# Kernel optimization log

Hardware: AMD Instinct MI355X
Metric: run time of the kernel (lower is better)

Reference implementation:

```python
import jax, jax.numpy as jnp
import numpy as np

NUM_HEADS = 8
NUM_GROUPS = 8
EPS = 1e-5


def group_norm(x, weight, bias):
    B, C, T, H, W = x.shape
    xg = x.reshape(B, NUM_GROUPS, C // NUM_GROUPS, T, H, W)
    mean = xg.mean(axis=(2, 3, 4, 5), keepdims=True)
    var = xg.var(axis=(2, 3, 4, 5), keepdims=True)
    xg = (xg - mean) * jax.lax.rsqrt(var + EPS)
    x = xg.reshape(B, C, T, H, W)
    return x * weight[None, :, None, None, None] + bias[None, :, None, None, None]


def setup_inputs() -> dict:
    key = jax.random.key(0)
    ks = jax.random.split(key, 5)
    B, C, T, H, W = 4, 512, 16, 32, 32
    x = jax.random.normal(ks[0], (B, C, T, H, W), dtype=jnp.float32)
    gn_weight = jnp.ones((C,), dtype=jnp.float32)
    gn_bias = jnp.zeros((C,), dtype=jnp.float32)
    # 1x1x1 Conv3d weights collapse to dense (out, in) matrices
    qkv_w = jax.random.normal(ks[1], (3 * C, C), dtype=jnp.float32) * (1.0 / np.sqrt(C))
    qkv_b = jax.random.normal(ks[2], (3 * C,), dtype=jnp.float32) * 0.02
    out_w = jax.random.normal(ks[3], (C, C), dtype=jnp.float32) * (1.0 / np.sqrt(C))
    out_b = jax.random.normal(ks[4], (C,), dtype=jnp.float32) * 0.02
    return {"x": x, "gn_weight": gn_weight, "gn_bias": gn_bias,
            "qkv_w": qkv_w, "qkv_b": qkv_b, "out_w": out_w, "out_b": out_b}


def reference(x, gn_weight, gn_bias, qkv_w, qkv_b, out_w, out_b):
    B, C, T, H, W = x.shape
    nh = NUM_HEADS
    d = C // nh
    N = T * H * W

    h = group_norm(x, gn_weight, gn_bias)

    # 1x1x1 conv == pointwise channel matmul
    hf = h.reshape(B, C, N)                                  # [B, C, N]
    qkv = jnp.einsum('oc,bcn->bon', qkv_w, hf) + qkv_b[None, :, None]
    q, k, v = jnp.split(qkv, 3, axis=1)                      # each [B, C, N]
    q = q.reshape(B, nh, d, N)
    k = k.reshape(B, nh, d, N)
    v = v.reshape(B, nh, d, N)

    # NOTE: faithful to the torch code — contraction is over N (tokens),
    # giving a [B, nh, d, d] channel-attention matrix; softmax over last d.
    scale = d ** (-0.5)
    attn = jnp.einsum('bhdn,bhen->bhde', q, k) * scale       # [B, nh, d, d]
    attn = jax.nn.softmax(attn, axis=-1)
    out = jnp.einsum('bhde,bhen->bhdn', attn, v)             # [B, nh, d, N]

    out = out.reshape(B, C, N)
    out = jnp.einsum('oc,bcn->bon', out_w, out) + out_b[None, :, None]
    out = out.reshape(B, C, T, H, W)
    return x + out
```

## Files before the change

### kernel.cpp

```cpp
#include <hip/hip_runtime.h>
#include <hip/hip_fp16.h>


#define CCH 512
#define NTOK 16384
#define NHEAD 8

typedef _Float16 f16;
typedef _Float16 f16x8 __attribute__((ext_vector_type(8)));
typedef float f32x4 __attribute__((ext_vector_type(4)));

__device__ __forceinline__ void g2l16(const void* g, void* l) {
  __builtin_amdgcn_global_load_lds((const __attribute__((address_space(1))) void*)g,
                                   (__attribute__((address_space(3))) void*)l,
                                   16, 0, 0);
}

__global__ __launch_bounds__(256) void k_cast2(const float* __restrict__ srcA,
                                               f16* __restrict__ dstA,
                                               const float* __restrict__ srcB,
                                               f16* __restrict__ dstB) {
  int i = blockIdx.x * 256 + threadIdx.x;
  int n4 = blockIdx.y ? (CCH * CCH / 4) : (3 * CCH * CCH / 4);
  const float* src = blockIdx.y ? srcB : srcA;
  f16* dst = blockIdx.y ? dstB : dstA;
  if (i < n4) {
    float4 v = *(const float4*)&src[i * 4];
    f16 h[4] __attribute__((aligned(8)));
    h[0] = (f16)v.x; h[1] = (f16)v.y; h[2] = (f16)v.z; h[3] = (f16)v.w;
    *(uint2*)&dst[i * 4] = *(const uint2*)h;
  }
}

__global__ __launch_bounds__(256) void k_wvt(const float* __restrict__ qkvw,
                                             f16* __restrict__ Wvt16) {
  int et = blockIdx.x, ct = blockIdx.y;
  __shared__ f16 tl[64][72];
  int t = threadIdx.x;
  int r = t >> 2, cq = (t & 3) * 16;
  const float* src = &qkvw[(size_t)(1024 + et * 64 + r) * CCH + ct * 64 + cq];
#pragma unroll
  for (int k = 0; k < 4; ++k) {
    float4 v = *(const float4*)(src + k * 4);
    tl[r][cq + k * 4 + 0] = (f16)v.x; tl[r][cq + k * 4 + 1] = (f16)v.y;
    tl[r][cq + k * 4 + 2] = (f16)v.z; tl[r][cq + k * 4 + 3] = (f16)v.w;
  }
  __syncthreads();
  f16 hv[16] __attribute__((aligned(16)));
#pragma unroll
  for (int j = 0; j < 16; ++j) hv[j] = tl[cq + j][r];
  f16* dst = &Wvt16[(size_t)(ct * 64 + r) * CCH + et * 64 + cq];
  *(uint4*)&dst[0] = ((const uint4*)hv)[0];
  *(uint4*)&dst[8] = ((const uint4*)hv)[1];
}

__global__ __launch_bounds__(256) void k_stats(const float* __restrict__ x,
                                               float* __restrict__ stats) {
  int bg = blockIdx.y;
  int chunk = blockIdx.x;
  const float4* p = (const float4*)(x + (size_t)bg * (64ull * NTOK)) + (size_t)chunk * 8192;
  float s = 0.f, q = 0.f;
  for (int i = threadIdx.x; i < 8192; i += 256) {
    float4 v = p[i];
    s += v.x + v.y + v.z + v.w;
    q += v.x * v.x + v.y * v.y + v.z * v.z + v.w * v.w;
  }
  for (int off = 32; off; off >>= 1) { s += __shfl_down(s, off); q += __shfl_down(q, off); }
  __shared__ float ls[4], lq[4];
  int wid = threadIdx.x >> 6, lane = threadIdx.x & 63;
  if (lane == 0) { ls[wid] = s; lq[wid] = q; }
  __syncthreads();
  if (threadIdx.x == 0) {
    atomicAdd(&stats[bg * 2 + 0], ls[0] + ls[1] + ls[2] + ls[3]);
    atomicAdd(&stats[bg * 2 + 1], lq[0] + lq[1] + lq[2] + lq[3]);
  }
}

__global__ __launch_bounds__(256) void k_gnorm(const float* __restrict__ x,
                                               const float* __restrict__ gw,
                                               const float* __restrict__ gb,
                                               const float* __restrict__ stats,
                                               f16* __restrict__ H, f16* __restrict__ Ht,
                                               float* __restrict__ svec) {
  int nc = blockIdx.x;
  int cg = blockIdx.y;
  int b = blockIdx.z;
  int t = threadIdx.x;
  __shared__ f16 T2[64][260];
  __shared__ float svp[4][64];
  float sum = stats[(b * 8 + cg) * 2], sq = stats[(b * 8 + cg) * 2 + 1];
  const float inv = 1.f / (64.f * (float)NTOK);
  float mean = sum * inv;
  float var = fmaxf(sq * inv - mean * mean, 0.f);
  float rsig = rsqrtf(var + 1e-5f);
  int c0 = cg * 64, n0 = nc * 256;
  int tq = t & 63, rr0 = t >> 6;
#pragma unroll
  for (int it = 0; it < 16; ++it) {
    int r = it * 4 + rr0;
    int c = c0 + r;
    float a = gw[c] * rsig;
    float bb = gb[c] - mean * a;
    size_t idx = ((size_t)(b * CCH + c)) * NTOK + n0 + tq * 4;
    float4 xv = *(const float4*)&x[idx];
    f16 hh[4] __attribute__((aligned(8)));
    hh[0] = (f16)(xv.x * a + bb);
    hh[1] = (f16)(xv.y * a + bb);
    hh[2] = (f16)(xv.z * a + bb);
    hh[3] = (f16)(xv.w * a + bb);
    *(uint2*)&H[idx] = *(const uint2*)hh;
    *(uint2*)&T2[r][tq * 4] = *(const uint2*)hh;
  }
  __syncthreads();
  {
    int c = t & 63, q = t >> 6;
    float acc = 0.f;
#pragma unroll
    for (int j = 0; j < 64; ++j) acc += (float)T2[c][q * 64 + j];
    svp[q][c] = acc;
  }
  __syncthreads();
  if (t < 64) {
    atomicAdd(&svec[b * CCH + c0 + t],
              svp[0][t] + svp[1][t] + svp[2][t] + svp[3][t]);
  }
  int s8 = t & 7, nl = t >> 3;
#pragma unroll
  for (int it = 0; it < 8; ++it) {
    int n = it * 32 + nl;
    f16 g[8] __attribute__((aligned(16)));
#pragma unroll
    for (int j = 0; j < 8; ++j) g[j] = T2[s8 * 8 + j][n];
    *(uint4*)&Ht[((size_t)b * NTOK + n0 + n) * CCH + c0 + s8 * 8] = *(const uint4*)g;
  }
}

#define SPLITS 16
__global__ __launch_bounds__(256, 2) void k_syrk(const f16* __restrict__ H,
                                                 float* __restrict__ G) {
  const int TI[10] = {0, 0, 0, 0, 1, 1, 1, 2, 2, 3};
  const int TJ[10] = {0, 1, 2, 3, 1, 2, 3, 2, 3, 3};
  int tile = blockIdx.x;
  int split = blockIdx.y;
  int b = blockIdx.z;
  int ii = TI[tile], jj = TJ[tile];
  int m0 = ii * 128, n0 = jj * 128;
  int t = threadIdx.x, lane = t & 63, wid = t >> 6;
  int wr = wid >> 1, wc = wid & 1;
  __shared__ __align__(16) f16 sA[128 * 64];
  __shared__ __align__(16) f16 sB[128 * 64];
  const f16* Hb = H + (size_t)b * CCH * NTOK;
  int k0 = split * (NTOK / SPLITS);
  f32x4 acc[4][4] = {};
  int ldsrow = wid * 8 + (lane >> 3);
  int slot = lane & 7;
  int lr = lane & 15, lk = lane >> 4;

  const int NS = (NTOK / SPLITS) / 64;
  for (int ks = 0; ks < NS; ++ks) {
    int kk0 = k0 + ks * 64;
    __syncthreads();
#pragma unroll
    for (int i = 0; i < 4; ++i) {
      int row = ldsrow + i * 32;
      int cA = ((slot ^ (row & 7)) * 8);
      g2l16(Hb + (size_t)(m0 + row) * NTOK + kk0 + cA, &sA[i * 2048 + wid * 512]);
      g2l16(Hb + (size_t)(n0 + row) * NTOK + kk0 + cA, &sB[i * 2048 + wid * 512]);
    }
    asm volatile("s_waitcnt vmcnt(0)" ::: "memory");
    __syncthreads();
#pragma unroll
    for (int kk = 0; kk < 2; ++kk) {
      f16x8 af[4], bf[4];
#pragma unroll
      for (int mi = 0; mi < 4; ++mi) {
        int row = wr * 64 + mi * 16 + lr;
        int ks8 = (kk * 4 + lk) ^ (row & 7);
        af[mi] = *(const f16x8*)&sA[row * 64 + ks8 * 8];
      }
#pragma unroll
      for (int ni = 0; ni < 4; ++ni) {
        int row = wc * 64 + ni * 16 + lr;
        int ks8 = (kk * 4 + lk) ^ (row & 7);
        bf[ni] = *(const f16x8*)&sB[row * 64 + ks8 * 8];
      }
#pragma unroll
      for (int mi = 0; mi < 4; ++mi)
#pragma unroll
        for (int ni = 0; ni < 4; ++ni)
          acc[mi][ni] = __builtin_amdgcn_mfma_f32_16x16x32_f16(af[mi], bf[ni], acc[mi][ni], 0, 0, 0);
    }
  }

  float* Gb = G + (size_t)b * CCH * CCH;
#pragma unroll
  for (int mi = 0; mi < 4; ++mi)
#pragma unroll
    for (int j = 0; j < 4; ++j) {
      int rr2 = m0 + wr * 64 + mi * 16 + lk * 4 + j;
#pragma unroll
      for (int ni = 0; ni < 4; ++ni) {
        int cc = n0 + wc * 64 + ni * 16 + lr;
        atomicAdd(&Gb[(size_t)rr2 * CCH + cc], acc[mi][ni][j]);
      }
    }
}

__global__ __launch_bounds__(256) void k_symm(float* __restrict__ G,
                                              f16* __restrict__ G16) {
  const int TI6[6] = {0, 0, 0, 1, 1, 2};
  const int TJ6[6] = {1, 2, 3, 2, 3, 3};
  int bx = blockIdx.x;
  int b = blockIdx.y;
  float* Gb = G + (size_t)b * CCH * CCH;
  f16* Gh = G16 + (size_t)b * CCH * CCH;
  __shared__ float s[64][65];
  int t = threadIdx.x;
  int r = t >> 2, cg = (t & 3) * 16;
  int ib, jb;
  bool mirror = bx < 24;
  if (mirror) {
    int t6 = bx >> 2, sub = bx & 3;
    ib = TI6[t6] * 2 + (sub >> 1); jb = TJ6[t6] * 2 + (sub & 1);
  } else {
    int idx = bx - 24; int dt = idx >> 2, sub = idx & 3;
    ib = dt * 2 + (sub >> 1); jb = dt * 2 + (sub & 1);
  }
  int grow = ib * 64 + r, gcol0 = jb * 64 + cg;
  const float* src = &Gb[(size_t)grow * CCH + gcol0];
  f16 hv[16] __attribute__((aligned(16)));
#pragma unroll
  for (int k = 0; k < 4; ++k) {
    float4 v = *(const float4*)(src + k * 4);
    if (mirror) {
      s[r][cg + k * 4 + 0] = v.x; s[r][cg + k * 4 + 1] = v.y;
      s[r][cg + k * 4 + 2] = v.z; s[r][cg + k * 4 + 3] = v.w;
    }
    hv[k * 4 + 0] = (f16)(v.x - ((grow == gcol0 + k * 4 + 0) ? 16384.f : 0.f));
    hv[k * 4 + 1] = (f16)(v.y - ((grow == gcol0 + k * 4 + 1) ? 16384.f : 0.f));
    hv[k * 4 + 2] = (f16)(v.z - ((grow == gcol0 + k * 4 + 2) ? 16384.f : 0.f));
    hv[k * 4 + 3] = (f16)(v.w - ((grow == gcol0 + k * 4 + 3) ? 16384.f : 0.f));
  }
  f16* d16 = &Gh[(size_t)grow * CCH + gcol0];
  *(uint4*)&d16[0] = ((const uint4*)hv)[0];
  *(uint4*)&d16[8] = ((const uint4*)hv)[1];
  if (mirror) {
    __syncthreads();
    float* dst = &Gb[(size_t)(jb * 64 + r) * CCH + ib * 64 + cg];
    f16 hw[16] __attribute__((aligned(16)));
#pragma unroll
    for (int k = 0; k < 4; ++k) {
      float4 v;
      v.x = s[cg + k * 4 + 0][r]; v.y = s[cg + k * 4 + 1][r];
      v.z = s[cg + k * 4 + 2][r]; v.w = s[cg + k * 4 + 3][r];
      *(float4*)(dst + k * 4) = v;
      hw[k * 4 + 0] = (f16)v.x; hw[k * 4 + 1] = (f16)v.y;
      hw[k * 4 + 2] = (f16)v.z; hw[k * 4 + 3] = (f16)v.w;
    }
    f16* m16 = &Gh[(size_t)(jb * 64 + r) * CCH + ib * 64 + cg];
    *(uint4*)&m16[0] = ((const uint4*)hw)[0];
    *(uint4*)&m16[8] = ((const uint4*)hw)[1];
  }
}

template <bool HALF_OUT, bool CORR>
__global__ __launch_bounds__(256, 2) void k_hgemm512(const f16* __restrict__ A16,
                                                     const f16* __restrict__ Bt16,
                                                     void* __restrict__ Cv,
                                                     const float* __restrict__ corr) {
  int n0 = blockIdx.x * 128, m0 = blockIdx.y * 128, b = blockIdx.z;
  int t = threadIdx.x, lane = t & 63, wid = t >> 6;
  int wr = wid >> 1, wc = wid & 1;
  __shared__ __align__(16) f16 sA[128 * 64];
  __shared__ __align__(16) f16 sB[128 * 64];
  const f16* A = A16;
  const f16* Bp = Bt16 + (size_t)b * CCH * CCH;
  f32x4 acc[4][4] = {};
  int ldsrow = wid * 8 + (lane >> 3);
  int slot = lane & 7;
  int lr = lane & 15, lk = lane >> 4;
  for (int ks = 0; ks < 8; ++ks) {
    int kk0 = ks * 64;
    __syncthreads();
#pragma unroll
    for (int i = 0; i < 4; ++i) {
      int row = ldsrow + i * 32;
      int cA = ((slot ^ (row & 7)) * 8);
      g2l16(A + (size_t)(m0 + row) * CCH + kk0 + cA, &sA[i * 2048 + wid * 512]);
      g2l16(Bp + (size_t)(n0 + row) * CCH + kk0 + cA, &sB[i * 2048 + wid * 512]);
    }
    asm volatile("s_waitcnt vmcnt(0)" ::: "memory");
    __syncthreads();
#pragma unroll
    for (int kk = 0; kk < 2; ++kk) {
      f16x8 af[4], bf[4];
#pragma unroll
      for (int mi = 0; mi < 4; ++mi) {
        int row = wr * 64 + mi * 16 + lr;
        int ks8 = (kk * 4 + lk) ^ (row & 7);
        af[mi] = *(const f16x8*)&sA[row * 64 + ks8 * 8];
      }
#pragma unroll
      for (int ni = 0; ni < 4; ++ni) {
        int row = wc * 64 + ni * 16 + lr;
        int ks8 = (kk * 4 + lk) ^ (row & 7);
        bf[ni] = *(const f16x8*)&sB[row * 64 + ks8 * 8];
      }
#pragma unroll
      for (int mi = 0; mi < 4; ++mi)
#pragma unroll
        for (int ni = 0; ni < 4; ++ni)
          acc[mi][ni] = __builtin_amdgcn_mfma_f32_16x16x32_f16(af[mi], bf[ni], acc[mi][ni], 0, 0, 0);
    }
  }
#pragma unroll
  for (int mi = 0; mi < 4; ++mi)
#pragma unroll
    for (int j = 0; j < 4; ++j) {
      int o = m0 + wr * 64 + mi * 16 + lk * 4 + j;
#pragma unroll
      for (int ni = 0; ni < 4; ++ni) {
        int n = n0 + wc * 64 + ni * 16 + lr;
        float v = acc[mi][ni][j];
        if constexpr (CORR) v += 16384.f * corr[(size_t)o * CCH + n];
        if constexpr (HALF_OUT)
          ((f16*)Cv)[(size_t)b * CCH * CCH + (size_t)o * CCH + n] = (f16)v;
        else
          ((float*)Cv)[(size_t)b * CCH * CCH + (size_t)o * CCH + n] = v;
      }
    }
}

__global__ __launch_bounds__(256) void k_attn(const f16* __restrict__ T1h,
                                              const f16* __restrict__ Wqkv16,
                                              const f16* __restrict__ Wvt16,
                                              const float* __restrict__ qkvw,
                                              const float* __restrict__ qkvb,
                                              const float* __restrict__ svec,
                                              f16* __restrict__ Rt16,
                                              float* __restrict__ pbv) {
  int h = blockIdx.x, b = blockIdx.y;
  int h64 = h * 64;
  int t = threadIdx.x, lane = t & 63, wid = t >> 6;
  int lr = lane & 15, lk = lane >> 4;
  __shared__ float ss[512];
  __shared__ float suq[64], suk[64], sbq[64], sbk[64], sbv[64];
  __shared__ float Lsm[64][68];
  __shared__ f16 Psm[64][72];

  for (int i = t; i < 512; i += 256) ss[i] = svec[b * CCH + i];
  if (t < 64) {
    sbq[t] = qkvb[h64 + t];
    sbk[t] = qkvb[512 + h64 + t];
    sbv[t] = qkvb[1024 + h64 + t];
  }
  __syncthreads();
  if (t < 128) {
    int o = t & 63; bool isk = t >= 64;
    const float* wr_ = qkvw + (size_t)((isk ? 512 : 0) + h64 + o) * CCH;
    float a = 0.f;
#pragma unroll
    for (int i = 0; i < 128; ++i) {
      float4 w = *(const float4*)&wr_[i * 4];
      a += w.x * ss[i * 4] + w.y * ss[i * 4 + 1] + w.z * ss[i * 4 + 2] + w.w * ss[i * 4 + 3];
    }
    (isk ? suk : suq)[o] = a;
  }
  int wr = wid >> 1, wc = wid & 1;
  f32x4 lacc[2][2] = {};
  const f16* Ab = T1h + (size_t)b * CCH * CCH;
  const f16* Bb = Wqkv16 + (size_t)(512 + h64) * CCH;
  for (int ks = 0; ks < 16; ++ks) {
    int kq = ks * 32 + lk * 8;
    f16x8 af[2], bf[2];
#pragma unroll
    for (int mi = 0; mi < 2; ++mi)
      af[mi] = *(const f16x8*)&Ab[(size_t)(h64 + wr * 32 + mi * 16 + lr) * CCH + kq];
#pragma unroll
    for (int ni = 0; ni < 2; ++ni)
      bf[ni] = *(const f16x8*)&Bb[(size_t)(wc * 32 + ni * 16 + lr) * CCH + kq];
#pragma unroll
    for (int mi = 0; mi < 2; ++mi)
#pragma unroll
      for (int ni = 0; ni < 2; ++ni)
        lacc[mi][ni] = __builtin_amdgcn_mfma_f32_16x16x32_f16(af[mi], bf[ni], lacc[mi][ni], 0, 0, 0);
  }
  __syncthreads();
#pragma unroll
  for (int mi = 0; mi < 2; ++mi)
#pragma unroll
    for (int ni = 0; ni < 2; ++ni)
#pragma unroll
      for (int j = 0; j < 4; ++j) {
        int d = wr * 32 + mi * 16 + lk * 4 + j;
        int e = wc * 32 + ni * 16 + lr;
        Lsm[d][e] = (lacc[mi][ni][j] + suq[d] * sbk[e] + sbq[d] * suk[e]
                     + 16384.f * sbq[d] * sbk[e]) * 0.125f;
      }
  __syncthreads();
  if (t < 64) {
    float m = -1e30f;
#pragma unroll
    for (int e = 0; e < 64; ++e) m = fmaxf(m, Lsm[t][e]);
    float p[64];
    float sum = 0.f;
#pragma unroll
    for (int e = 0; e < 64; ++e) { p[e] = expf(Lsm[t][e] - m); sum += p[e]; }
    float r = 1.f / sum, pb = 0.f;
#pragma unroll
    for (int e = 0; e < 64; ++e) {
      float pv = p[e] * r;
      Psm[t][e] = (f16)pv;
      pb += pv * sbv[e];
    }
    pbv[b * CCH + h64 + t] = pb;
  }
  __syncthreads();
  f32x4 acc[4][8] = {};
  int c0w = wid * 128;
#pragma unroll
  for (int kk = 0; kk < 2; ++kk) {
    int e0 = kk * 32 + lk * 8;
    f16x8 pa[4], wb[8];
#pragma unroll
    for (int mi = 0; mi < 4; ++mi)
      pa[mi] = *(const f16x8*)&Psm[mi * 16 + lr][e0];
#pragma unroll
    for (int ni = 0; ni < 8; ++ni)
      wb[ni] = *(const f16x8*)&Wvt16[(size_t)(c0w + ni * 16 + lr) * CCH + h64 + e0];
#pragma unroll
    for (int mi = 0; mi < 4; ++mi)
#pragma unroll
      for (int ni = 0; ni < 8; ++ni)
        acc[mi][ni] = __builtin_amdgcn_mfma_f32_16x16x32_f16(pa[mi], wb[ni], acc[mi][ni], 0, 0, 0);
  }
#pragma unroll
  for (int mi = 0; mi < 4; ++mi)
#pragma unroll
    for (int ni = 0; ni < 8; ++ni) {
      int d0 = mi * 16 + lk * 4;
      int c = c0w + ni * 16 + lr;
      f16 hv[4] __attribute__((aligned(8)));
#pragma unroll
      for (int j = 0; j < 4; ++j) hv[j] = (f16)acc[mi][ni][j];
      *(uint2*)&Rt16[((size_t)b * CCH + c) * CCH + h64 + d0] = *(const uint2*)hv;
    }
}

__global__ __launch_bounds__(256) void k_cvec(const float* __restrict__ outw,
                                              const float* __restrict__ outb,
                                              const float* __restrict__ pbv,
                                              float* __restrict__ cvec) {
  int o = blockIdx.x * 64 + (threadIdx.x >> 2);
  int l = threadIdx.x & 3;
  int b = blockIdx.y;
  __shared__ float sp[512];
  for (int i = threadIdx.x; i < 512; i += 256) sp[i] = pbv[b * CCH + i];
  __syncthreads();
  const float* wr_ = outw + (size_t)o * CCH + l * 128;
  const float* spp = sp + l * 128;
  float a = 0.f;
#pragma unroll
  for (int i = 0; i < 32; ++i) {
    float4 w = *(const float4*)&wr_[i * 4];
    a += w.x * spp[i * 4] + w.y * spp[i * 4 + 1] + w.z * spp[i * 4 + 2] + w.w * spp[i * 4 + 3];
  }
  a += __shfl_down(a, 2);
  a += __shfl_down(a, 1);
  if (l == 0) cvec[b * CCH + o] = a + outb[o];
}

__global__ __launch_bounds__(256, 2) void k_out(const f16* __restrict__ M16,
                                                const f16* __restrict__ Ht,
                                                const float* __restrict__ x,
                                                const float* __restrict__ cvec,
                                                float* __restrict__ out) {
  int nt = blockIdx.x;
  int mt = blockIdx.y;
  int b = blockIdx.z;
  int m0 = mt * 128, n0 = nt * 128;
  int t = threadIdx.x, lane = t & 63, wid = t >> 6;
  int wr = wid >> 1, wc = wid & 1;
  __shared__ __align__(16) f16 sA[128 * 64];
  __shared__ __align__(16) f16 sB[128 * 64];
  const f16* A = M16 + (size_t)b * CCH * CCH;
  const f16* Bp = Ht + (size_t)b * NTOK * CCH;
  f32x4 acc[4][4] = {};
  int ldsrow = wid * 8 + (lane >> 3);
  int slot = lane & 7;
  int lr = lane & 15, lk = lane >> 4;
  for (int ks = 0; ks < 8; ++ks) {
    int kk0 = ks * 64;
    __syncthreads();
#pragma unroll
    for (int i = 0; i < 4; ++i) {
      int row = ldsrow + i * 32;
      int cA = ((slot ^ (row & 7)) * 8);
      g2l16(A + (size_t)(m0 + row) * CCH + kk0 + cA, &sA[i * 2048 + wid * 512]);
      g2l16(Bp + (size_t)(n0 + row) * CCH + kk0 + cA, &sB[i * 2048 + wid * 512]);
    }
    asm volatile("s_waitcnt vmcnt(0)" ::: "memory");
    __syncthreads();
#pragma unroll
    for (int kk = 0; kk < 2; ++kk) {
      f16x8 af[4], bf[4];
#pragma unroll
      for (int mi = 0; mi < 4; ++mi) {
        int row = wr * 64 + mi * 16 + lr;
        int ks8 = (kk * 4 + lk) ^ (row & 7);
        af[mi] = *(const f16x8*)&sA[row * 64 + ks8 * 8];
      }
#pragma unroll
      for (int ni = 0; ni < 4; ++ni) {
        int row = wc * 64 + ni * 16 + lr;
        int ks8 = (kk * 4 + lk) ^ (row & 7);
        bf[ni] = *(const f16x8*)&sB[row * 64 + ks8 * 8];
      }
#pragma unroll
      for (int mi = 0; mi < 4; ++mi)
#pragma unroll
        for (int ni = 0; ni < 4; ++ni)
          acc[mi][ni] = __builtin_amdgcn_mfma_f32_16x16x32_f16(bf[ni], af[mi], acc[mi][ni], 0, 0, 0);
    }
  }

  const float* xb = x + ((size_t)b * CCH) * NTOK;
  float* ob = out + ((size_t)b * CCH) * NTOK;
#pragma unroll
  for (int mi = 0; mi < 4; ++mi) {
    int o = m0 + wr * 64 + mi * 16 + lr;
    float cv = cvec[b * CCH + o];
    size_t rowoff = (size_t)o * NTOK;
#pragma unroll
    for (int ni = 0; ni < 4; ++ni) {
      int n = n0 + wc * 64 + ni * 16 + lk * 4;
      float4 xv = *(const float4*)&xb[rowoff + n];
      float4 ov;
      ov.x = xv.x + acc[mi][ni][0] + cv;
      ov.y = xv.y + acc[mi][ni][1] + cv;
      ov.z = xv.z + acc[mi][ni][2] + cv;
      ov.w = xv.w + acc[mi][ni][3] + cv;
      *(float4*)&ob[rowoff + n] = ov;
    }
  }
}

extern "C" void kernel_launch(void* const* d_in, const int* in_sizes, int n_in,
                              void* d_out, int out_size, void* d_ws, size_t ws_size,
                              hipStream_t stream) {
  const float* x    = (const float*)d_in[0];
  const float* gw   = (const float*)d_in[1];
  const float* gb   = (const float*)d_in[2];
  const float* qkvw = (const float*)d_in[3];
  const float* qkvb = (const float*)d_in[4];
  const float* outw = (const float*)d_in[5];
  const float* outb = (const float*)d_in[6];
  int B = in_sizes[0] / (CCH * NTOK);

  char* ws = (char*)d_ws;
  size_t off = 0;
  f16* H      = (f16*)(ws + off);   off += (size_t)B * CCH * NTOK * 2;
  f16* Ht     = (f16*)(ws + off);   off += (size_t)B * NTOK * CCH * 2;
  float* G    = (float*)(ws + off); off += (size_t)B * CCH * CCH * 4;
  f16* G16    = (f16*)(ws + off);   off += (size_t)B * CCH * CCH * 2;
  f16* T1h    = (f16*)(ws + off);   off += (size_t)B * CCH * CCH * 2;
  f16* Rt16   = (f16*)(ws + off);   off += (size_t)B * CCH * CCH * 2;
  f16* M16    = (f16*)(ws + off);   off += (size_t)B * CCH * CCH * 2;
  f16* Wqkv16 = (f16*)(ws + off);   off += (size_t)3 * CCH * CCH * 2;
  f16* Ow16   = (f16*)(ws + off);   off += (size_t)CCH * CCH * 2;
  f16* Wvt16  = (f16*)(ws + off);   off += (size_t)CCH * CCH * 2;
  float* pbv  = (float*)(ws + off); off += (size_t)B * CCH * 4;
  float* cvec = (float*)(ws + off); off += (size_t)B * CCH * 4;
  float* stats = (float*)(ws + off); off += (size_t)B * 8 * 2 * 4;
  float* svec  = (float*)(ws + off); off += (size_t)B * CCH * 4;
  size_t zbytes = (size_t)(B * 8 * 2 + B * CCH) * 4;

  hipMemsetAsync(G, 0, (size_t)B * CCH * CCH * 4, stream);
  hipMemsetAsync(stats, 0, zbytes, stream);

  k_cast2<<<dim3(3 * CCH * CCH / 1024, 2), 256, 0, stream>>>(qkvw, Wqkv16, outw, Ow16);
  k_wvt<<<dim3(8, 8), 256, 0, stream>>>(qkvw, Wvt16);
  k_stats<<<dim3(32, B * 8), 256, 0, stream>>>(x, stats);
  k_gnorm<<<dim3(64, 8, B), 256, 0, stream>>>(x, gw, gb, stats, H, Ht, svec);
  k_syrk<<<dim3(10, SPLITS, B), 256, 0, stream>>>(H, G);
  k_symm<<<dim3(40, B), 256, 0, stream>>>(G, G16);
  k_hgemm512<true, true><<<dim3(4, 4, B), 256, 0, stream>>>(Wqkv16, G16, T1h, qkvw);
  k_attn<<<dim3(NHEAD, B), 256, 0, stream>>>(T1h, Wqkv16, Wvt16, qkvw, qkvb, svec,
                                             Rt16, pbv);
  k_hgemm512<true, false><<<dim3(4, 4, B), 256, 0, stream>>>(Ow16, Rt16, M16, nullptr);
  k_cvec<<<dim3(8, B), 256, 0, stream>>>(outw, outb, pbv, cvec);
  k_out<<<dim3(128, 4, B), 256, 0, stream>>>(M16, Ht, x, cvec, (float*)d_out);
}
```

Baseline: 302.7 us.

## Merge prep kernels and fuse middle stages into one persistent kernel with grid barriers

Combines the weight casts, V-weight transpose and group-norm stats into one launch, and fuses the Gram symmetrize, the two 512x512 GEMMs, attention softmax and the cvec stage into a single 64-block persistent kernel. The stages are separated by atomic-counter grid barriers. This removes several small kernel launches and their inter-kernel gaps. The cost is that the 64-block grid assumes B=4 and that all blocks are co-resident, and the spin barriers add sync overhead.

```diff
diff --git a/kernel.cpp b/kernel.cpp
--- a/kernel.cpp
+++ b/kernel.cpp
@@ -16,63 +16,72 @@
                                    16, 0, 0);
 }
 
-__global__ __launch_bounds__(256) void k_cast2(const float* __restrict__ srcA,
-                                               f16* __restrict__ dstA,
-                                               const float* __restrict__ srcB,
-                                               f16* __restrict__ dstB) {
-  int i = blockIdx.x * 256 + threadIdx.x;
-  int n4 = blockIdx.y ? (CCH * CCH / 4) : (3 * CCH * CCH / 4);
-  const float* src = blockIdx.y ? srcB : srcA;
-  f16* dst = blockIdx.y ? dstB : dstA;
-  if (i < n4) {
+__device__ __forceinline__ void gbar(int* bar, int id, int nblk) {
+  __syncthreads();
+  if (threadIdx.x == 0) {
+    __hip_atomic_fetch_add(&bar[id], 1, __ATOMIC_RELEASE, __HIP_MEMORY_SCOPE_AGENT);
+    while (__hip_atomic_load(&bar[id], __ATOMIC_ACQUIRE, __HIP_MEMORY_SCOPE_AGENT) < nblk)
+      __builtin_amdgcn_s_sleep(2);
+  }
+  __syncthreads();
+}
+
+__global__ __launch_bounds__(256) void k_prep(const float* __restrict__ x,
+                                              float* __restrict__ stats,
+                                              const float* __restrict__ qkvw,
+                                              f16* __restrict__ Wqkv16,
+                                              const float* __restrict__ outw,
+                                              f16* __restrict__ Ow16,
+                                              f16* __restrict__ Wvt16) {
+  __shared__ __align__(16) char smp[9216];
+  int bid = blockIdx.x;
+  int t = threadIdx.x;
+  if (bid < 1024) {
+    int chunk = bid & 31, bg = bid >> 5;
+    const float4* p = (const float4*)(x + (size_t)bg * (64ull * NTOK)) + (size_t)chunk * 8192;
+    float s = 0.f, q = 0.f;
+    for (int i = t; i < 8192; i += 256) {
+      float4 v = p[i];
+      s += v.x + v.y + v.z + v.w;
+      q += v.x * v.x + v.y * v.y + v.z * v.z + v.w * v.w;
+    }
+    for (int off = 32; off; off >>= 1) { s += __shfl_down(s, off); q += __shfl_down(q, off); }
+    float* ls = (float*)smp; float* lq = ls + 4;
+    int wid = t >> 6, lane = t & 63;
+    if (lane == 0) { ls[wid] = s; lq[wid] = q; }
+    __syncthreads();
+    if (t == 0) {
+      atomicAdd(&stats[bg * 2 + 0], ls[0] + ls[1] + ls[2] + ls[3]);
+      atomicAdd(&stats[bg * 2 + 1], lq[0] + lq[1] + lq[2] + lq[3]);
+    }
+  } else if (bid < 2048) {
+    bool isB = bid >= 1792;
+    int i = (isB ? (bid - 1792) : (bid - 1024)) * 256 + t;
+    const float* src = isB ? outw : qkvw;
+    f16* dst = isB ? Ow16 : Wqkv16;
     float4 v = *(const float4*)&src[i * 4];
     f16 h[4] __attribute__((aligned(8)));
     h[0] = (f16)v.x; h[1] = (f16)v.y; h[2] = (f16)v.z; h[3] = (f16)v.w;
     *(uint2*)&dst[i * 4] = *(const uint2*)h;
-  }
-}
-
-__global__ __launch_bounds__(256) void k_wvt(const float* __restrict__ qkvw,
-                                             f16* __restrict__ Wvt16) {
-  int et = blockIdx.x, ct = blockIdx.y;
-  __shared__ f16 tl[64][72];
-  int t = threadIdx.x;
-  int r = t >> 2, cq = (t & 3) * 16;
-  const float* src = &qkvw[(size_t)(1024 + et * 64 + r) * CCH + ct * 64 + cq];
-#pragma unroll
-  for (int k = 0; k < 4; ++k) {
-    float4 v = *(const float4*)(src + k * 4);
-    tl[r][cq + k * 4 + 0] = (f16)v.x; tl[r][cq + k * 4 + 1] = (f16)v.y;
-    tl[r][cq + k * 4 + 2] = (f16)v.z; tl[r][cq + k * 4 + 3] = (f16)v.w;
-  }
-  __syncthreads();
-  f16 hv[16] __attribute__((aligned(16)));
-#pragma unroll
-  for (int j = 0; j < 16; ++j) hv[j] = tl[cq + j][r];
-  f16* dst = &Wvt16[(size_t)(ct * 64 + r) * CCH + et * 64 + cq];
-  *(uint4*)&dst[0] = ((const uint4*)hv)[0];
-  *(uint4*)&dst[8] = ((const uint4*)hv)[1];
-}
-
-__global__ __launch_bounds__(256) void k_stats(const float* __restrict__ x,
-                                               float* __restrict__ stats) {
-  int bg = blockIdx.y;
-  int chunk = blockIdx.x;
-  const float4* p = (const float4*)(x + (size_t)bg * (64ull * NTOK)) + (size_t)chunk * 8192;
-  float s = 0.f, q = 0.f;
-  for (int i = threadIdx.x; i < 8192; i += 256) {
-    float4 v = p[i];
-    s += v.x + v.y + v.z + v.w;
-    q += v.x * v.x + v.y * v.y + v.z * v.z + v.w * v.w;
-  }
-  for (int off = 32; off; off >>= 1) { s += __shfl_down(s, off); q += __shfl_down(q, off); }
-  __shared__ float ls[4], lq[4];
-  int wid = threadIdx.x >> 6, lane = threadIdx.x & 63;
-  if (lane == 0) { ls[wid] = s; lq[wid] = q; }
-  __syncthreads();
-  if (threadIdx.x == 0) {
-    atomicAdd(&stats[bg * 2 + 0], ls[0] + ls[1] + ls[2] + ls[3]);
-    atomicAdd(&stats[bg * 2 + 1], lq[0] + lq[1] + lq[2] + lq[3]);
+  } else {
+    int j = bid - 2048;
+    int et = j >> 3, ct = j & 7;
+    f16 (*tl)[72] = (f16(*)[72])smp;
+    int r = t >> 2, cq = (t & 3) * 16;
+    const float* src = &qkvw[(size_t)(1024 + et * 64 + r) * CCH + ct * 64 + cq];
+#pragma unroll
+    for (int k = 0; k < 4; ++k) {
+      float4 v = *(const float4*)(src + k * 4);
+      tl[r][cq + k * 4 + 0] = (f16)v.x; tl[r][cq + k * 4 + 1] = (f16)v.y;
+      tl[r][cq + k * 4 + 2] = (f16)v.z; tl[r][cq + k * 4 + 3] = (f16)v.w;
+    }
+    __syncthreads();
+    f16 hv[16] __attribute__((aligned(16)));
+#pragma unroll
+    for (int jj = 0; jj < 16; ++jj) hv[jj] = tl[cq + jj][r];
+    f16* dst = &Wvt16[(size_t)(ct * 64 + r) * CCH + et * 64 + cq];
+    *(uint4*)&dst[0] = ((const uint4*)hv)[0];
+    *(uint4*)&dst[8] = ((const uint4*)hv)[1];
   }
 }
 
@@ -206,74 +215,16 @@
     }
 }
 
-__global__ __launch_bounds__(256) void k_symm(float* __restrict__ G,
-                                              f16* __restrict__ G16) {
-  const int TI6[6] = {0, 0, 0, 1, 1, 2};
-  const int TJ6[6] = {1, 2, 3, 2, 3, 3};
-  int bx = blockIdx.x;
-  int b = blockIdx.y;
-  float* Gb = G + (size_t)b * CCH * CCH;
-  f16* Gh = G16 + (size_t)b * CCH * CCH;
-  __shared__ float s[64][65];
-  int t = threadIdx.x;
-  int r = t >> 2, cg = (t & 3) * 16;
-  int ib, jb;
-  bool mirror = bx < 24;
-  if (mirror) {
-    int t6 = bx >> 2, sub = bx & 3;
-    ib = TI6[t6] * 2 + (sub >> 1); jb = TJ6[t6] * 2 + (sub & 1);
-  } else {
-    int idx = bx - 24; int dt = idx >> 2, sub = idx & 3;
-    ib = dt * 2 + (sub >> 1); jb = dt * 2 + (sub & 1);
-  }
-  int grow = ib * 64 + r, gcol0 = jb * 64 + cg;
-  const float* src = &Gb[(size_t)grow * CCH + gcol0];
-  f16 hv[16] __attribute__((aligned(16)));
-#pragma unroll
-  for (int k = 0; k < 4; ++k) {
-    float4 v = *(const float4*)(src + k * 4);
-    if (mirror) {
-      s[r][cg + k * 4 + 0] = v.x; s[r][cg + k * 4 + 1] = v.y;
-      s[r][cg + k * 4 + 2] = v.z; s[r][cg + k * 4 + 3] = v.w;
-    }
-    hv[k * 4 + 0] = (f16)(v.x - ((grow == gcol0 + k * 4 + 0) ? 16384.f : 0.f));
-    hv[k * 4 + 1] = (f16)(v.y - ((grow == gcol0 + k * 4 + 1) ? 16384.f : 0.f));
-    hv[k * 4 + 2] = (f16)(v.z - ((grow == gcol0 + k * 4 + 2) ? 16384.f : 0.f));
-    hv[k * 4 + 3] = (f16)(v.w - ((grow == gcol0 + k * 4 + 3) ? 16384.f : 0.f));
-  }
-  f16* d16 = &Gh[(size_t)grow * CCH + gcol0];
-  *(uint4*)&d16[0] = ((const uint4*)hv)[0];
-  *(uint4*)&d16[8] = ((const uint4*)hv)[1];
-  if (mirror) {
-    __syncthreads();
-    float* dst = &Gb[(size_t)(jb * 64 + r) * CCH + ib * 64 + cg];
-    f16 hw[16] __attribute__((aligned(16)));
-#pragma unroll
-    for (int k = 0; k < 4; ++k) {
-      float4 v;
-      v.x = s[cg + k * 4 + 0][r]; v.y = s[cg + k * 4 + 1][r];
-      v.z = s[cg + k * 4 + 2][r]; v.w = s[cg + k * 4 + 3][r];
-      *(float4*)(dst + k * 4) = v;
-      hw[k * 4 + 0] = (f16)v.x; hw[k * 4 + 1] = (f16)v.y;
-      hw[k * 4 + 2] = (f16)v.z; hw[k * 4 + 3] = (f16)v.w;
-    }
-    f16* m16 = &Gh[(size_t)(jb * 64 + r) * CCH + ib * 64 + cg];
-    *(uint4*)&m16[0] = ((const uint4*)hw)[0];
-    *(uint4*)&m16[8] = ((const uint4*)hw)[1];
-  }
-}
-
-template <bool HALF_OUT, bool CORR>
-__global__ __launch_bounds__(256, 2) void k_hgemm512(const f16* __restrict__ A16,
-                                                     const f16* __restrict__ Bt16,
-                                                     void* __restrict__ Cv,
-                                                     const float* __restrict__ corr) {
-  int n0 = blockIdx.x * 128, m0 = blockIdx.y * 128, b = blockIdx.z;
+template <bool CORR>
+__device__ __forceinline__ void hgemm_tile(const f16* __restrict__ A16,
+                                           const f16* __restrict__ Bt16,
+                                           f16* __restrict__ Cv,
+                                           const float* __restrict__ corr,
+                                           int m0, int n0, int b, char* sm) {
   int t = threadIdx.x, lane = t & 63, wid = t >> 6;
   int wr = wid >> 1, wc = wid & 1;
-  __shared__ __align__(16) f16 sA[128 * 64];
-  __shared__ __align__(16) f16 sB[128 * 64];
-  const f16* A = A16;
+  f16* sA = (f16*)sm;
+  f16* sB = (f16*)(sm + 16384);
   const f16* Bp = Bt16 + (size_t)b * CCH * CCH;
   f32x4 acc[4][4] = {};
   int ldsrow = wid * 8 + (lane >> 3);
@@ -286,7 +237,7 @@
     for (int i = 0; i < 4; ++i) {
       int row = ldsrow + i * 32;
       int cA = ((slot ^ (row & 7)) * 8);
-      g2l16(A + (size_t)(m0 + row) * CCH + kk0 + cA, &sA[i * 2048 + wid * 512]);
+      g2l16(A16 + (size_t)(m0 + row) * CCH + kk0 + cA, &sA[i * 2048 + wid * 512]);
       g2l16(Bp + (size_t)(n0 + row) * CCH + kk0 + cA, &sB[i * 2048 + wid * 512]);
     }
     asm volatile("s_waitcnt vmcnt(0)" ::: "memory");
@@ -323,151 +274,235 @@
         int n = n0 + wc * 64 + ni * 16 + lr;
         float v = acc[mi][ni][j];
         if constexpr (CORR) v += 16384.f * corr[(size_t)o * CCH + n];
-        if constexpr (HALF_OUT)
-          ((f16*)Cv)[(size_t)b * CCH * CCH + (size_t)o * CCH + n] = (f16)v;
-        else
-          ((float*)Cv)[(size_t)b * CCH * CCH + (size_t)o * CCH + n] = v;
-      }
-    }
-}
-
-__global__ __launch_bounds__(256) void k_attn(const f16* __restrict__ T1h,
-                                              const f16* __restrict__ Wqkv16,
-                                              const f16* __restrict__ Wvt16,
-                                              const float* __restrict__ qkvw,
-                                              const float* __restrict__ qkvb,
-                                              const float* __restrict__ svec,
-                                              f16* __restrict__ Rt16,
-                                              float* __restrict__ pbv) {
-  int h = blockIdx.x, b = blockIdx.y;
-  int h64 = h * 64;
-  int t = threadIdx.x, lane = t & 63, wid = t >> 6;
-  int lr = lane & 15, lk = lane >> 4;
-  __shared__ float ss[512];
-  __shared__ float suq[64], suk[64], sbq[64], sbk[64], sbv[64];
-  __shared__ float Lsm[64][68];
-  __shared__ f16 Psm[64][72];
-
-  for (int i = t; i < 512; i += 256) ss[i] = svec[b * CCH + i];
-  if (t < 64) {
-    sbq[t] = qkvb[h64 + t];
-    sbk[t] = qkvb[512 + h64 + t];
-    sbv[t] = qkvb[1024 + h64 + t];
-  }
-  __syncthreads();
-  if (t < 128) {
-    int o = t & 63; bool isk = t >= 64;
-    const float* wr_ = qkvw + (size_t)((isk ? 512 : 0) + h64 + o) * CCH;
+        Cv[(size_t)b * CCH * CCH + (size_t)o * CCH + n] = (f16)v;
+      }
+    }
+}
+
+__global__ __launch_bounds__(256) void k_mid(float* __restrict__ G,
+                                             f16* __restrict__ G16,
+                                             const f16* __restrict__ Wqkv16,
+                                             f16* __restrict__ T1h,
+                                             const float* __restrict__ qkvw,
+                                             const float* __restrict__ qkvb,
+                                             const float* __restrict__ svec,
+                                             const f16* __restrict__ Wvt16,
+                                             f16* __restrict__ Rt16,
+                                             float* __restrict__ pbv,
+                                             const f16* __restrict__ Ow16,
+                                             f16* __restrict__ M16,
+                                             const float* __restrict__ outw,
+                                             const float* __restrict__ outb,
+                                             float* __restrict__ cvec,
+                                             int* __restrict__ bar, int B) {
+  __shared__ __align__(16) char sm[32768];
+  const int NB = 64;
+  int bid = blockIdx.x;
+  int t = threadIdx.x;
+
+  {
+    const int TI6[6] = {0, 0, 0, 1, 1, 2};
+    const int TJ6[6] = {1, 2, 3, 2, 3, 3};
+    float (*s)[65] = (float(*)[65])sm;
+    int r = t >> 2, cg = (t & 3) * 16;
+    for (int it = bid; it < 40 * B; it += NB) {
+      int bx = it % 40, b = it / 40;
+      float* Gb = G + (size_t)b * CCH * CCH;
+      f16* Gh = G16 + (size_t)b * CCH * CCH;
+      int ib, jb;
+      bool mirror = bx < 24;
+      if (mirror) {
+        int t6 = bx >> 2, sub = bx & 3;
+        ib = TI6[t6] * 2 + (sub >> 1); jb = TJ6[t6] * 2 + (sub & 1);
+      } else {
+        int idx = bx - 24; int dt = idx >> 2, sub = idx & 3;
+        ib = dt * 2 + (sub >> 1); jb = dt * 2 + (sub & 1);
+      }
+      int grow = ib * 64 + r, gcol0 = jb * 64 + cg;
+      const float* src = &Gb[(size_t)grow * CCH + gcol0];
+      f16 hv[16] __attribute__((aligned(16)));
+#pragma unroll
+      for (int k = 0; k < 4; ++k) {
+        float4 v = *(const float4*)(src + k * 4);
+        if (mirror) {
+          s[r][cg + k * 4 + 0] = v.x; s[r][cg + k * 4 + 1] = v.y;
+          s[r][cg + k * 4 + 2] = v.z; s[r][cg + k * 4 + 3] = v.w;
+        }
+        hv[k * 4 + 0] = (f16)(v.x - ((grow == gcol0 + k * 4 + 0) ? 16384.f : 0.f));
+        hv[k * 4 + 1] = (f16)(v.y - ((grow == gcol0 + k * 4 + 1) ? 16384.f : 0.f));
+        hv[k * 4 + 2] = (f16)(v.z - ((grow == gcol0 + k * 4 + 2) ? 16384.f : 0.f));
+        hv[k * 4 + 3] = (f16)(v.w - ((grow == gcol0 + k * 4 + 3) ? 16384.f : 0.f));
+      }
+      f16* d16 = &Gh[(size_t)grow * CCH + gcol0];
+      *(uint4*)&d16[0] = ((const uint4*)hv)[0];
+      *(uint4*)&d16[8] = ((const uint4*)hv)[1];
+      if (mirror) {
+        __syncthreads();
+        float* dst = &Gb[(size_t)(jb * 64 + r) * CCH + ib * 64 + cg];
+        f16 hw[16] __attribute__((aligned(16)));
+#pragma unroll
+        for (int k = 0; k < 4; ++k) {
+          float4 v;
+          v.x = s[cg + k * 4 + 0][r]; v.y = s[cg + k * 4 + 1][r];
+          v.z = s[cg + k * 4 + 2][r]; v.w = s[cg + k * 4 + 3][r];
+          *(float4*)(dst + k * 4) = v;
+          hw[k * 4 + 0] = (f16)v.x; hw[k * 4 + 1] = (f16)v.y;
+          hw[k * 4 + 2] = (f16)v.z; hw[k * 4 + 3] = (f16)v.w;
+        }
+        f16* m16p = &Gh[(size_t)(jb * 64 + r) * CCH + ib * 64 + cg];
+        *(uint4*)&m16p[0] = ((const uint4*)hw)[0];
+        *(uint4*)&m16p[8] = ((const uint4*)hw)[1];
+      }
+      __syncthreads();
+    }
+  }
+  gbar(bar, 0, NB);
+
+  {
+    int n0 = (bid & 3) * 128, m0 = ((bid >> 2) & 3) * 128, b = bid >> 4;
+    hgemm_tile<true>(Wqkv16, G16, T1h, qkvw, m0, n0, b, sm);
+  }
+  gbar(bar, 1, NB);
+
+  if (bid < NHEAD * B) {
+    int h = bid & 7, b = bid >> 3;
+    int h64 = h * 64;
+    int lane = t & 63, wid = t >> 6;
+    int lr = lane & 15, lk = lane >> 4;
+    float* ss = (float*)sm;
+    float* suq = ss + 512;
+    float* suk = suq + 64;
+    float* sbq = suk + 64;
+    float* sbk = sbq + 64;
+    float* sbv = sbk + 64;
+    float (*Lsm)[68] = (float(*)[68])(sm + 3328);
+    f16 (*Psm)[72] = (f16(*)[72])(sm + 3328 + 17408);
+
+    for (int i = t; i < 512; i += 256) ss[i] = svec[b * CCH + i];
+    if (t < 64) {
+      sbq[t] = qkvb[h64 + t];
+      sbk[t] = qkvb[512 + h64 + t];
+      sbv[t] = qkvb[1024 + h64 + t];
+    }
+    __syncthreads();
+    if (t < 128) {
+      int o = t & 63; bool isk = t >= 64;
+      const float* wr_ = qkvw + (size_t)((isk ? 512 : 0) + h64 + o) * CCH;
+      float a = 0.f;
+#pragma unroll
+      for (int i = 0; i < 128; ++i) {
+        float4 w = *(const float4*)&wr_[i * 4];
+        a += w.x * ss[i * 4] + w.y * ss[i * 4 + 1] + w.z * ss[i * 4 + 2] + w.w * ss[i * 4 + 3];
+      }
+      (isk ? suk : suq)[o] = a;
+    }
+    int wr = wid >> 1, wc = wid & 1;
+    f32x4 lacc[2][2] = {};
+    const f16* Ab = T1h + (size_t)b * CCH * CCH;
+    const f16* Bb = Wqkv16 + (size_t)(512 + h64) * CCH;
+    for (int ks = 0; ks < 16; ++ks) {
+      int kq = ks * 32 + lk * 8;
+      f16x8 af[2], bf[2];
+#pragma unroll
+      for (int mi = 0; mi < 2; ++mi)
+        af[mi] = *(const f16x8*)&Ab[(size_t)(h64 + wr * 32 + mi * 16 + lr) * CCH + kq];
+#pragma unroll
+      for (int ni = 0; ni < 2; ++ni)
+        bf[ni] = *(const f16x8*)&Bb[(size_t)(wc * 32 + ni * 16 + lr) * CCH + kq];
+#pragma unroll
+      for (int mi = 0; mi < 2; ++mi)
+#pragma unroll
+        for (int ni = 0; ni < 2; ++ni)
+          lacc[mi][ni] = __builtin_amdgcn_mfma_f32_16x16x32_f16(af[mi], bf[ni], lacc[mi][ni], 0, 0, 0);
+    }
+    __syncthreads();
+#pragma unroll
+    for (int mi = 0; mi < 2; ++mi)
+#pragma unroll
+      for (int ni = 0; ni < 2; ++ni)
+#pragma unroll
+        for (int j = 0; j < 4; ++j) {
+          int d = wr * 32 + mi * 16 + lk * 4 + j;
+          int e = wc * 32 + ni * 16 + lr;
+          Lsm[d][e] = (lacc[mi][ni][j] + suq[d] * sbk[e] + sbq[d] * suk[e]
+                       + 16384.f * sbq[d] * sbk[e]) * 0.125f;
+        }
+    __syncthreads();
+    if (t < 64) {
+      float m = -1e30f;
+#pragma unroll
+      for (int e = 0; e < 64; ++e) m = fmaxf(m, Lsm[t][e]);
+      float p[64];
+      float sum = 0.f;
+#pragma unroll
+      for (int e = 0; e < 64; ++e) { p[e] = expf(Lsm[t][e] - m); sum += p[e]; }
+      float r = 1.f / sum, pb = 0.f;
+#pragma unroll
+      for (int e = 0; e < 64; ++e) {
+        float pv = p[e] * r;
+        Psm[t][e] = (f16)pv;
+        pb += pv * sbv[e];
+      }
+      pbv[b * CCH + h64 + t] = pb;
+    }
+    __syncthreads();
+    f32x4 acc[4][8] = {};
+    int c0w = wid * 128;
+#pragma unroll
+    for (int kk = 0; kk < 2; ++kk) {
+      int e0 = kk * 32 + lk * 8;
+      f16x8 pa[4], wb[8];
+#pragma unroll
+      for (int mi = 0; mi < 4; ++mi)
+        pa[mi] = *(const f16x8*)&Psm[mi * 16 + lr][e0];
+#pragma unroll
+      for (int ni = 0; ni < 8; ++ni)
+        wb[ni] = *(const f16x8*)&Wvt16[(size_t)(c0w + ni * 16 + lr) * CCH + h64 + e0];
+#pragma unroll
+      for (int mi = 0; mi < 4; ++mi)
+#pragma unroll
+        for (int ni = 0; ni < 8; ++ni)
+          acc[mi][ni] = __builtin_amdgcn_mfma_f32_16x16x32_f16(pa[mi], wb[ni], acc[mi][ni], 0, 0, 0);
+    }
+#pragma unroll
+    for (int mi = 0; mi < 4; ++mi)
+#pragma unroll
+      for (int ni = 0; ni < 8; ++ni) {
+        int d0 = mi * 16 + lk * 4;
+        int c = c0w + ni * 16 + lr;
+        f16 hv[4] __attribute__((aligned(8)));
+#pragma unroll
+        for (int j = 0; j < 4; ++j) hv[j] = (f16)acc[mi][ni][j];
+        *(uint2*)&Rt16[((size_t)b * CCH + c) * CCH + h64 + d0] = *(const uint2*)hv;
+      }
+  }
+  gbar(bar, 2, NB);
+
+  {
+    int n0 = (bid & 3) * 128, m0 = ((bid >> 2) & 3) * 128, b = bid >> 4;
+    hgemm_tile<false>(Ow16, Rt16, M16, nullptr, m0, n0, b, sm);
+  }
+  gbar(bar, 3, NB);
+
+  if (bid < 8 * B) {
+    int ob = bid & 7, b = bid >> 3;
+    float* sp = (float*)sm;
+    for (int i = t; i < 512; i += 256) sp[i] = pbv[b * CCH + i];
+    __syncthreads();
+    int o = ob * 64 + (t >> 2);
+    int l = t & 3;
+    const float* wr_ = outw + (size_t)o * CCH + l * 128;
+    const float* spp = sp + l * 128;
     float a = 0.f;
 #pragma unroll
-    for (int i = 0; i < 128; ++i) {
+    for (int i = 0; i < 32; ++i) {
       float4 w = *(const float4*)&wr_[i * 4];
-      a += w.x * ss[i * 4] + w.y * ss[i * 4 + 1] + w.z * ss[i * 4 + 2] + w.w * ss[i * 4 + 3];
-    }
-    (isk ? suk : suq)[o] = a;
-  }
-  int wr = wid >> 1, wc = wid & 1;
-  f32x4 lacc[2][2] = {};
-  const f16* Ab = T1h + (size_t)b * CCH * CCH;
-  const f16* Bb = Wqkv16 + (size_t)(512 + h64) * CCH;
-  for (int ks = 0; ks < 16; ++ks) {
-    int kq = ks * 32 + lk * 8;
-    f16x8 af[2], bf[2];
-#pragma unroll
-    for (int mi = 0; mi < 2; ++mi)
-      af[mi] = *(const f16x8*)&Ab[(size_t)(h64 + wr * 32 + mi * 16 + lr) * CCH + kq];
-#pragma unroll
-    for (int ni = 0; ni < 2; ++ni)
-      bf[ni] = *(const f16x8*)&Bb[(size_t)(wc * 32 + ni * 16 + lr) * CCH + kq];
-#pragma unroll
-    for (int mi = 0; mi < 2; ++mi)
-#pragma unroll
-      for (int ni = 0; ni < 2; ++ni)
-        lacc[mi][ni] = __builtin_amdgcn_mfma_f32_16x16x32_f16(af[mi], bf[ni], lacc[mi][ni], 0, 0, 0);
-  }
-  __syncthreads();
-#pragma unroll
-  for (int mi = 0; mi < 2; ++mi)
-#pragma unroll
-    for (int ni = 0; ni < 2; ++ni)
-#pragma unroll
-      for (int j = 0; j < 4; ++j) {
-        int d = wr * 32 + mi * 16 + lk * 4 + j;
-        int e = wc * 32 + ni * 16 + lr;
-        Lsm[d][e] = (lacc[mi][ni][j] + suq[d] * sbk[e] + sbq[d] * suk[e]
-                     + 16384.f * sbq[d] * sbk[e]) * 0.125f;
-      }
-  __syncthreads();
-  if (t < 64) {
-    float m = -1e30f;
-#pragma unroll
-    for (int e = 0; e < 64; ++e) m = fmaxf(m, Lsm[t][e]);
-    float p[64];
-    float sum = 0.f;
-#pragma unroll
-    for (int e = 0; e < 64; ++e) { p[e] = expf(Lsm[t][e] - m); sum += p[e]; }
-    float r = 1.f / sum, pb = 0.f;
-#pragma unroll
-    for (int e = 0; e < 64; ++e) {
-      float pv = p[e] * r;
-      Psm[t][e] = (f16)pv;
-      pb += pv * sbv[e];
-    }
-    pbv[b * CCH + h64 + t] = pb;
-  }
-  __syncthreads();
-  f32x4 acc[4][8] = {};
-  int c0w = wid * 128;
-#pragma unroll
-  for (int kk = 0; kk < 2; ++kk) {
-    int e0 = kk * 32 + lk * 8;
-    f16x8 pa[4], wb[8];
-#pragma unroll
-    for (int mi = 0; mi < 4; ++mi)
-      pa[mi] = *(const f16x8*)&Psm[mi * 16 + lr][e0];
-#pragma unroll
-    for (int ni = 0; ni < 8; ++ni)
-      wb[ni] = *(const f16x8*)&Wvt16[(size_t)(c0w + ni * 16 + lr) * CCH + h64 + e0];
-#pragma unroll
-    for (int mi = 0; mi < 4; ++mi)
-#pragma unroll
-      for (int ni = 0; ni < 8; ++ni)
-        acc[mi][ni] = __builtin_amdgcn_mfma_f32_16x16x32_f16(pa[mi], wb[ni], acc[mi][ni], 0, 0, 0);
-  }
-#pragma unroll
-  for (int mi = 0; mi < 4; ++mi)
-#pragma unroll
-    for (int ni = 0; ni < 8; ++ni) {
-      int d0 = mi * 16 + lk * 4;
-      int c = c0w + ni * 16 + lr;
-      f16 hv[4] __attribute__((aligned(8)));
-#pragma unroll
-      for (int j = 0; j < 4; ++j) hv[j] = (f16)acc[mi][ni][j];
-      *(uint2*)&Rt16[((size_t)b * CCH + c) * CCH + h64 + d0] = *(const uint2*)hv;
-    }
-}
-
-__global__ __launch_bounds__(256) void k_cvec(const float* __restrict__ outw,
-                                              const float* __restrict__ outb,
-                                              const float* __restrict__ pbv,
-                                              float* __restrict__ cvec) {
-  int o = blockIdx.x * 64 + (threadIdx.x >> 2);
-  int l = threadIdx.x & 3;
-  int b = blockIdx.y;
-  __shared__ float sp[512];
-  for (int i = threadIdx.x; i < 512; i += 256) sp[i] = pbv[b * CCH + i];
-  __syncthreads();
-  const float* wr_ = outw + (size_t)o * CCH + l * 128;
-  const float* spp = sp + l * 128;
-  float a = 0.f;
-#pragma unroll
-  for (int i = 0; i < 32; ++i) {
-    float4 w = *(const float4*)&wr_[i * 4];
-    a += w.x * spp[i * 4] + w.y * spp[i * 4 + 1] + w.z * spp[i * 4 + 2] + w.w * spp[i * 4 + 3];
-  }
-  a += __shfl_down(a, 2);
-  a += __shfl_down(a, 1);
-  if (l == 0) cvec[b * CCH + o] = a + outb[o];
+      a += w.x * spp[i * 4] + w.y * spp[i * 4 + 1] + w.z * spp[i * 4 + 2] + w.w * spp[i * 4 + 3];
+    }
+    a += __shfl_down(a, 2);
+    a += __shfl_down(a, 1);
+    if (l == 0) cvec[b * CCH + o] = a + outb[o];
+  }
 }
 
 __global__ __launch_bounds__(256, 2) void k_out(const f16* __restrict__ M16,
@@ -573,21 +608,17 @@
   float* cvec = (float*)(ws + off); off += (size_t)B * CCH * 4;
   float* stats = (float*)(ws + off); off += (size_t)B * 8 * 2 * 4;
   float* svec  = (float*)(ws + off); off += (size_t)B * CCH * 4;
-  size_t zbytes = (size_t)(B * 8 * 2 + B * CCH) * 4;
+  int* bar     = (int*)(ws + off);   off += 8 * 4;
+  size_t zbytes = (size_t)(B * 8 * 2 + B * CCH + 8) * 4;
 
   hipMemsetAsync(G, 0, (size_t)B * CCH * CCH * 4, stream);
   hipMemsetAsync(stats, 0, zbytes, stream);
 
-  k_cast2<<<dim3(3 * CCH * CCH / 1024, 2), 256, 0, stream>>>(qkvw, Wqkv16, outw, Ow16);
-  k_wvt<<<dim3(8, 8), 256, 0, stream>>>(qkvw, Wvt16);
-  k_stats<<<dim3(32, B * 8), 256, 0, stream>>>(x, stats);
+  k_prep<<<dim3(2112), 256, 0, stream>>>(x, stats, qkvw, Wqkv16, outw, Ow16, Wvt16);
   k_gnorm<<<dim3(64, 8, B), 256, 0, stream>>>(x, gw, gb, stats, H, Ht, svec);
   k_syrk<<<dim3(10, SPLITS, B), 256, 0, stream>>>(H, G);
-  k_symm<<<dim3(40, B), 256, 0, stream>>>(G, G16);
-  k_hgemm512<true, true><<<dim3(4, 4, B), 256, 0, stream>>>(Wqkv16, G16, T1h, qkvw);
-  k_attn<<<dim3(NHEAD, B), 256, 0, stream>>>(T1h, Wqkv16, Wvt16, qkvw, qkvb, svec,
-                                             Rt16, pbv);
-  k_hgemm512<true, false><<<dim3(4, 4, B), 256, 0, stream>>>(Ow16, Rt16, M16, nullptr);
-  k_cvec<<<dim3(8, B), 256, 0, stream>>>(outw, outb, pbv, cvec);
+  k_mid<<<dim3(64), 256, 0, stream>>>(G, G16, Wqkv16, T1h, qkvw, qkvb, svec,
+                                      Wvt16, Rt16, pbv, Ow16, M16,
+                                      outw, outb, cvec, bar, B);
   k_out<<<dim3(128, 4, B), 256, 0, stream>>>(M16, Ht, x, cvec, (float*)d_out);
 }
```

Result: slower. 322.7 us (+6.6%).
